# Kernel optimization log

Hardware: AMD Instinct MI355X
Metric: run time of the kernel (lower is better)

Reference implementation:

```python
import jax, jax.numpy as jnp
import numpy as np

N = 8192
C = 128
K = 20          # neighbors per dilation branch
DILS = (1, 2)   # dilations
K_FULL = K * max(DILS)  # neighbors in the base knn graph
R = 4           # upsampling ratio
N_IDGCN = 2     # inception blocks
NEG_SLOPE_CONV = 0.2
NEG_SLOPE_MLP = 0.01  # torch LeakyReLU default in reconstructor


def knn_idx(pos, k):
    # brute-force knn on [N,3]; exclude self by taking k+1 and dropping col 0
    sq = jnp.sum(pos * pos, axis=-1)                       # [N]
    d = sq[:, None] + sq[None, :] - 2.0 * (pos @ pos.T)    # [N,N]
    _, idx = jax.lax.top_k(-d, k + 1)                      # nearest first
    return idx[:, 1:]                                      # [N,k]


def edge_conv(x, idx, W, b):
    # EdgeConv: max_j LeakyReLU(W @ [x_i, x_j - x_i] + b)
    xj = x[idx]                                            # [N,k,C] gather
    xi = jnp.broadcast_to(x[:, None, :], xj.shape)
    e = jnp.concatenate([xi, xj - xi], axis=-1)            # [N,k,2C]
    h = jax.nn.leaky_relu(e @ W + b, NEG_SLOPE_CONV)
    return jnp.max(h, axis=1)                              # [N,Cout]


def setup_inputs() -> dict:
    key = jax.random.key(0)
    ks = jax.random.split(key, 10)
    s_lift = 1.0 / np.sqrt(6.0)
    s_gcn = 1.0 / np.sqrt(2.0 * C)
    s_mlp = 1.0 / np.sqrt(C)
    n_gcn = N_IDGCN * len(DILS)
    return {
        "x": jax.random.normal(ks[0], (N, 3), dtype=jnp.float32),
        "W0": jax.random.normal(ks[1], (6, C), dtype=jnp.float32) * s_lift,
        "b0": jnp.zeros((C,), dtype=jnp.float32),
        "Wg": jax.random.normal(ks[2], (n_gcn, 2 * C, C), dtype=jnp.float32) * s_gcn,
        "bg": jnp.zeros((n_gcn, C), dtype=jnp.float32),
        "Wu": jax.random.normal(ks[3], (2 * C, R * C), dtype=jnp.float32) * s_gcn,
        "bu": jnp.zeros((R * C,), dtype=jnp.float32),
        "Wr1": jax.random.normal(ks[4], (C, C), dtype=jnp.float32) * s_mlp,
        "br1": jnp.zeros((C,), dtype=jnp.float32),
        "Wr2": jax.random.normal(ks[5], (C, 3), dtype=jnp.float32) * s_mlp,
        "br2": jnp.zeros((3,), dtype=jnp.float32),
    }


def reference(x, W0, b0, Wg, bg, Wu, bu, Wr1, br1, Wr2, br2):
    pos = x
    # knn graph on positions (k * max(dilations) neighbors)
    idx = knn_idx(pos, K_FULL)                             # [N, K_FULL]
    # lift 3 -> C with an EdgeConv on the first K neighbors
    h = edge_conv(pos, idx[:, :K], W0, b0)                 # [N, C]
    # Inception DenseGCN feature extractor: dilated EdgeConv branches + residual
    li = 0
    for _ in range(N_IDGCN):
        acc = jnp.zeros_like(h)
        for d in DILS:
            idx_d = idx[:, ::d][:, :K]                     # dilated neighbors
            acc = acc + edge_conv(h, idx_d, Wg[li], bg[li])
            li += 1
        h = h + acc / float(len(DILS))                     # residual
    # NodeShuffle upsampler: EdgeConv to r*C then shuffle nodes
    u = edge_conv(h, idx[:, :K], Wu, bu)                   # [N, r*C]
    u = u.reshape(N * R, C)                                # [N*r, C]
    # reconstructor MLP -> 3D coordinates
    q = jax.nn.leaky_relu(u @ Wr1 + br1, NEG_SLOPE_MLP)
    q = q @ Wr2 + br2                                      # [N*r, 3]
    return q
```

## Files before the change

### kernel.cpp

```cpp
#include <hip/hip_runtime.h>
#include <math.h>

#define N_PTS 8192
#define KFULL 40
#define KNB 20
#define QB 8
#define KBLK 512
#define NBUCK 1024
#define CAP 384

typedef unsigned short u16;
typedef unsigned int u32;
typedef unsigned long long u64;
typedef __attribute__((ext_vector_type(8))) short bf16x8;
typedef __attribute__((ext_vector_type(4))) float f32x4;

__device__ __forceinline__ u16 f2b(float v) {
  u32 u = __float_as_uint(v);
  return (u16)((u + 0x7FFFu + ((u >> 16) & 1u)) >> 16);
}
__device__ __forceinline__ u32 pk2(float a, float b) {
  return (u32)f2b(a) | ((u32)f2b(b) << 16);
}
__device__ __forceinline__ u32 dmap(float d) {
  u32 b = __float_as_uint(d);
  return b ^ ((u32)(((int)b) >> 31) | 0x80000000u);
}
__device__ __forceinline__ void maxu4(const uint4 v, float m[8]) {
  m[0] = fmaxf(m[0], __uint_as_float(v.x << 16));
  m[1] = fmaxf(m[1], __uint_as_float(v.x & 0xFFFF0000u));
  m[2] = fmaxf(m[2], __uint_as_float(v.y << 16));
  m[3] = fmaxf(m[3], __uint_as_float(v.y & 0xFFFF0000u));
  m[4] = fmaxf(m[4], __uint_as_float(v.z << 16));
  m[5] = fmaxf(m[5], __uint_as_float(v.z & 0xFFFF0000u));
  m[6] = fmaxf(m[6], __uint_as_float(v.w << 16));
  m[7] = fmaxf(m[7], __uint_as_float(v.w & 0xFFFF0000u));
}
__device__ __forceinline__ void unp4(const uint4 v, float p[8]) {
  p[0] = __uint_as_float(v.x << 16);
  p[1] = __uint_as_float(v.x & 0xFFFF0000u);
  p[2] = __uint_as_float(v.y << 16);
  p[3] = __uint_as_float(v.y & 0xFFFF0000u);
  p[4] = __uint_as_float(v.z << 16);
  p[5] = __uint_as_float(v.z & 0xFFFF0000u);
  p[6] = __uint_as_float(v.w << 16);
  p[7] = __uint_as_float(v.w & 0xFFFF0000u);
}

typedef const __attribute__((address_space(1))) unsigned int* gas_p;
typedef __attribute__((address_space(3))) unsigned int* las_p;
__device__ __forceinline__ void gll16(const void* g, void* l) {
  __builtin_amdgcn_global_load_lds((gas_p)g, (las_p)l, 16, 0, 0);
}

__device__ __forceinline__ void scan_cut(const u32 (*hist)[NBUCK], int* s_cut,
                                         int t) {
  const int w = t >> 6, lane = t & 63;
  if (w < QB / 2) {
    const u32* H = hist[w];
    const int base = lane * (NBUCK / 64);
    u32 lsum = 0;
#pragma unroll
    for (int k = 0; k < NBUCK / 64; ++k) lsum += H[base + k];
    u32 inc = lsum;
#pragma unroll
    for (int off = 1; off < 64; off <<= 1) {
      const u32 u = __shfl_up(inc, off);
      if (lane >= off) inc += u;
    }
    const u32 excl = inc - lsum;
    const u32 TGT = KFULL + 1;
    const u32 exlo = excl & 0xFFFFu, inlo = inc & 0xFFFFu;
    if (exlo < TGT && inlo >= TGT) {
      u32 cum = exlo;
      for (int k = 0; k < NBUCK / 64; ++k) {
        cum += H[base + k] & 0xFFFFu;
        if (cum >= TGT) { s_cut[2 * w] = base + k; break; }
      }
    }
    const u32 exhi = excl >> 16, inhi = inc >> 16;
    if (exhi < TGT && inhi >= TGT) {
      u32 cum = exhi;
      for (int k = 0; k < NBUCK / 64; ++k) {
        cum += H[base + k] >> 16;
        if (cum >= TGT) { s_cut[2 * w + 1] = base + k; break; }
      }
    }
  }
}

__global__ __launch_bounds__(KBLK) void knn_kernel(const float4* __restrict__ pos4,
                                                   int* __restrict__ idx_out) {
  __shared__ __align__(16) u32 hmem[CAP * QB * 2];
  u32 (*hist)[NBUCK] = (u32(*)[NBUCK])hmem;
  u64 (*cand)[CAP] = (u64(*)[CAP])hmem;
  __shared__ float4 s_q[QB];
  __shared__ int s_cut[QB];
  __shared__ int s_cnt[QB];

  const int qb = blockIdx.x * QB, t = threadIdx.x;
  if (t < QB) {
    s_q[t] = pos4[qb + t];
    s_cnt[t] = 0;
  }
  for (int b = t; b < 4 * NBUCK; b += KBLK) hmem[b] = 0;
  __syncthreads();

  float qx[QB], qy[QB], qz[QB], qs[QB];
#pragma unroll
  for (int q = 0; q < QB; ++q) {
    const float4 v = s_q[q];
    qx[q] = -2.0f * v.x; qy[q] = -2.0f * v.y; qz[q] = -2.0f * v.z; qs[q] = v.w;
  }

  {
    const int j = t << 4;
    const float4 p = pos4[j];
#pragma unroll
    for (int q = 0; q < QB; ++q) {
      const float d = fmaf(qx[q], p.x, fmaf(qy[q], p.y, fmaf(qz[q], p.z, qs[q] + p.w)));
      const u32 bk = dmap(d) >> 22;
      atomicAdd(&hist[q >> 1][bk], 1u << ((q & 1) * 16));
    }
  }
  __syncthreads();
  scan_cut(hist, s_cut, t);
  __syncthreads();
  int bcut[QB];
#pragma unroll
  for (int q = 0; q < QB; ++q) bcut[q] = s_cut[q];
  for (int b = t; b < 4 * NBUCK; b += KBLK) hmem[b] = 0;
  __syncthreads();

#pragma unroll 2
  for (int s = 0; s < 16; ++s) {
    const int j = t + (s << 9);
    const float4 p = pos4[j];
#pragma unroll
    for (int q = 0; q < QB; ++q) {
      const float d = fmaf(qx[q], p.x, fmaf(qy[q], p.y, fmaf(qz[q], p.z, qs[q] + p.w)));
      const u32 bk = dmap(d) >> 22;
      if ((int)bk <= bcut[q]) atomicAdd(&hist[q >> 1][bk], 1u << ((q & 1) * 16));
    }
  }
  __syncthreads();
  scan_cut(hist, s_cut, t);
  __syncthreads();
#pragma unroll
  for (int q = 0; q < QB; ++q) bcut[q] = s_cut[q];
  __syncthreads();

#pragma unroll 2
  for (int s = 0; s < 16; ++s) {
    const int j = t + (s << 9);
    const float4 p = pos4[j];
#pragma unroll
    for (int q = 0; q < QB; ++q) {
      const float d = fmaf(qx[q], p.x, fmaf(qy[q], p.y, fmaf(qz[q], p.z, qs[q] + p.w)));
      const u32 mp = dmap(d);
      if ((int)(mp >> 22) <= bcut[q]) {
        const int slot = atomicAdd(&s_cnt[q], 1);
        if (slot < CAP) cand[q][slot] = ((u64)mp << 13) | (u64)j;
      }
    }
  }
  __syncthreads();

  {
    const int w = t >> 6, lane = t & 63;
    const int cnt = s_cnt[w] < CAP ? s_cnt[w] : CAP;
    for (int c0 = lane; c0 < cnt; c0 += 64) {
      const u64 my = cand[w][c0];
      int rank = 0;
      for (int c = 0; c < cnt; ++c) rank += (cand[w][c] < my) ? 1 : 0;
      if (rank >= 1 && rank <= KFULL)
        idx_out[(qb + w) * KFULL + (rank - 1)] = (int)(my & 0x1FFFull);
    }
  }
}

__device__ __forceinline__ void wcvt_body(const float* __restrict__ src,
                                          u16* __restrict__ dst, int ncols,
                                          int rows_per_tensor, int elems_per_tensor,
                                          int rg, int k) {
  const int li = rg / rows_per_tensor;
  const int r = rg % rows_per_tensor;
  const float* s = src + (size_t)li * elems_per_tensor;
  u16* d = dst + (size_t)li * elems_per_tensor;
  const int part = r / ncols, col = r % ncols;
  d[(size_t)r * 128 + k] = f2b(s[(size_t)(part * 128 + k) * ncols + col]);
}

__global__ __launch_bounds__(128) void prep_kernel(
    const float* __restrict__ x, const float* __restrict__ W0,
    const float* __restrict__ b0, const float* __restrict__ Wg,
    const float* __restrict__ Wu, const float* __restrict__ Wr1,
    float* __restrict__ Aout, u16* __restrict__ Pout, u16* __restrict__ Wgb,
    u16* __restrict__ Wub, u16* __restrict__ Wr1b, float4* __restrict__ pos4) {
  const int b = blockIdx.x, t = threadIdx.x;
  if (b < 8192) {
    const float px = x[b * 3 + 0], py = x[b * 3 + 1], pz = x[b * 3 + 2];
    const float a = b0[t] + px * W0[t] + py * W0[128 + t] + pz * W0[256 + t];
    const float p = px * W0[384 + t] + py * W0[512 + t] + pz * W0[640 + t];
    Aout[(size_t)b * 128 + t] = a;
    Pout[(size_t)b * 128 + t] = f2b(p);
  } else if (b < 9216) {
    wcvt_body(Wg, Wgb, 128, 256, 256 * 128, b - 8192, t);
  } else if (b < 10240) {
    wcvt_body(Wu, Wub, 512, 1024, 1024 * 128, b - 9216, t);
  } else if (b < 10368) {
    wcvt_body(Wr1, Wr1b, 128, 128, 128 * 128, b - 10240, t);
  } else {
    const int j = (b - 10368) * 128 + t;
    const float px = x[j * 3 + 0], py = x[j * 3 + 1], pz = x[j * 3 + 2];
    pos4[j] = make_float4(px, py, pz, px * px + py * py + pz * pz);
  }
}

__global__ __launch_bounds__(256) void gemm_mfma_kernel(
    const u16* __restrict__ Ain, const u16* __restrict__ Wt,
    const float* __restrict__ bias, int GA, int span_shift, int nAtot, int nPtot,
    float slope, int use_act, float* __restrict__ Aout, u16* __restrict__ Pout) {
  __shared__ __align__(16) u16 Al[128 * 128];
  __shared__ __align__(16) u16 Bl[64 * 128];
  const int bm = blockIdx.x * 128;
  const int bn = blockIdx.y * 64;
  const int tid = threadIdx.x;

#pragma unroll
  for (int it = 0; it < 8; ++it) {
    const int g = it * 256 + tid;
    const int row = g >> 4, cc = g & 15;
    const int sc = cc ^ (row & 7);
    gll16(Ain + (size_t)(bm + row) * 128 + sc * 8, &Al[g * 8]);
  }
#pragma unroll
  for (int it = 0; it < 4; ++it) {
    const int g = it * 256 + tid;
    const int row = g >> 4, cc = g & 15;
    const int sc = cc ^ (row & 7);
    gll16(Wt + (size_t)(bn + row) * 128 + sc * 8, &Bl[g * 8]);
  }
  __syncthreads();

  const int wv = tid >> 6, lane = tid & 63;
  const int wm = wv & 1, wn = wv >> 1;
  const int lr = lane & 15, lk = lane >> 4;

  bf16x8 a[4][4], b[2][4];
  f32x4 acc[4][2];
#pragma unroll
  for (int m = 0; m < 4; ++m)
#pragma unroll
    for (int n = 0; n < 2; ++n) acc[m][n] = (f32x4){0.f, 0.f, 0.f, 0.f};

#pragma unroll
  for (int m = 0; m < 4; ++m) {
    const int row = wm * 64 + m * 16 + lr;
#pragma unroll
    for (int ks = 0; ks < 4; ++ks) {
      const int c = ks * 4 + lk;
      a[m][ks] = *(const bf16x8*)&Al[row * 128 + (c ^ (row & 7)) * 8];
    }
  }
#pragma unroll
  for (int n = 0; n < 2; ++n) {
    const int col = wn * 32 + n * 16 + lr;
#pragma unroll
    for (int ks = 0; ks < 4; ++ks) {
      const int c = ks * 4 + lk;
      b[n][ks] = *(const bf16x8*)&Bl[col * 128 + (c ^ (col & 7)) * 8];
    }
  }

#pragma unroll
  for (int ks = 0; ks < 4; ++ks)
#pragma unroll
    for (int m = 0; m < 4; ++m)
#pragma unroll
      for (int n = 0; n < 2; ++n)
        acc[m][n] = __builtin_amdgcn_mfma_f32_16x16x32_bf16(a[m][ks], b[n][ks],
                                                            acc[m][n], 0, 0, 0);

  const int span = 1 << span_shift;
  const int GP = span - GA;
#pragma unroll
  for (int n = 0; n < 2; ++n) {
    const int col = bn + wn * 32 + n * 16 + lr;
    const int g = col >> span_shift;
    const int wi = col & (span - 1);
    const bool isA = wi < GA;
    const float bv = isA ? bias[g * GA + wi] : 0.f;
#pragma unroll
    for (int m = 0; m < 4; ++m) {
      const int row0 = bm + wm * 64 + m * 16 + lk * 4;
#pragma unroll
      for (int r = 0; r < 4; ++r) {
        float v = acc[m][n][r] + bv;
        if (isA) {
          if (use_act) v = v > 0.f ? v : v * slope;
          Aout[(size_t)(row0 + r) * nAtot + g * GA + wi] = v;
        } else {
          Pout[(size_t)(row0 + r) * nPtot + g * GP + (wi - GA)] = f2b(v);
        }
      }
    }
  }
}

__global__ __launch_bounds__(256) void gather_one_kernel(
    const float* __restrict__ A, const u16* __restrict__ P,
    const int* __restrict__ idx, int C, int dil, float* __restrict__ outf,
    u16* __restrict__ outb) {
  const int t = threadIdx.x;
  const int i = blockIdx.x * 16 + (t >> 4);
  const int c = blockIdx.y * 128 + (t & 15) * 8;
  float m[8];
#pragma unroll
  for (int k = 0; k < 8; ++k) m[k] = -INFINITY;
  const int ib = i * KFULL;
#pragma unroll
  for (int j = 0; j < KNB; ++j) {
    const int n = idx[ib + j * dil] & (N_PTS - 1);
    maxu4(*(const uint4*)&P[(size_t)n * C + c], m);
  }
  float pv[8];
  unp4(*(const uint4*)&P[(size_t)i * C + c], pv);
  const float4 a0 = *(const float4*)&A[(size_t)i * C + c];
  const float4 a1 = *(const float4*)&A[(size_t)i * C + c + 4];
  const float av[8] = {a0.x, a0.y, a0.z, a0.w, a1.x, a1.y, a1.z, a1.w};
  float v[8];
#pragma unroll
  for (int k = 0; k < 8; ++k) {
    const float x = av[k] - pv[k] + m[k];
    v[k] = x > 0.f ? x : 0.2f * x;
  }
  if (outf) {
    *(float4*)&outf[(size_t)i * C + c] = make_float4(v[0], v[1], v[2], v[3]);
    *(float4*)&outf[(size_t)i * C + c + 4] = make_float4(v[4], v[5], v[6], v[7]);
  }
  if (outb) {
    uint4 pb = {pk2(v[0], v[1]), pk2(v[2], v[3]), pk2(v[4], v[5]), pk2(v[6], v[7])};
    *(uint4*)&outb[(size_t)i * C + c] = pb;
  }
}

__global__ __launch_bounds__(256) void gather_pair_kernel(
    const float* __restrict__ Ap, const u16* __restrict__ Pp,
    const int* __restrict__ idx, float* __restrict__ h, u16* __restrict__ hb) {
  const int t = threadIdx.x;
  const int i = blockIdx.x * 16 + (t >> 4);
  const int c = (t & 15) * 8;
  float m1[8], m2[8];
#pragma unroll
  for (int k = 0; k < 8; ++k) { m1[k] = -INFINITY; m2[k] = -INFINITY; }
  const int ib = i * KFULL;
#pragma unroll
  for (int j = 0; j < KNB; ++j) {
    const int n1 = idx[ib + j] & (N_PTS - 1);
    maxu4(*(const uint4*)&Pp[(size_t)n1 * 256 + c], m1);
    const int n2 = idx[ib + 2 * j] & (N_PTS - 1);
    maxu4(*(const uint4*)&Pp[(size_t)n2 * 256 + 128 + c], m2);
  }
  float p0[8], p1[8];
  unp4(*(const uint4*)&Pp[(size_t)i * 256 + c], p0);
  unp4(*(const uint4*)&Pp[(size_t)i * 256 + 128 + c], p1);
  const float4 a00 = *(const float4*)&Ap[(size_t)i * 256 + c];
  const float4 a01 = *(const float4*)&Ap[(size_t)i * 256 + c + 4];
  const float4 a10 = *(const float4*)&Ap[(size_t)i * 256 + 128 + c];
  const float4 a11 = *(const float4*)&Ap[(size_t)i * 256 + 128 + c + 4];
  const float av0[8] = {a00.x, a00.y, a00.z, a00.w, a01.x, a01.y, a01.z, a01.w};
  const float av1[8] = {a10.x, a10.y, a10.z, a10.w, a11.x, a11.y, a11.z, a11.w};
  const float4 h0 = *(const float4*)&h[(size_t)i * 128 + c];
  const float4 h1 = *(const float4*)&h[(size_t)i * 128 + c + 4];
  const float hv[8] = {h0.x, h0.y, h0.z, h0.w, h1.x, h1.y, h1.z, h1.w};
  float v[8];
#pragma unroll
  for (int k = 0; k < 8; ++k) {
    float x1 = av0[k] - p0[k] + m1[k];
    x1 = x1 > 0.f ? x1 : 0.2f * x1;
    float x2 = av1[k] - p1[k] + m2[k];
    x2 = x2 > 0.f ? x2 : 0.2f * x2;
    v[k] = hv[k] + 0.5f * (x1 + x2);
  }
  *(float4*)&h[(size_t)i * 128 + c] = make_float4(v[0], v[1], v[2], v[3]);
  *(float4*)&h[(size_t)i * 128 + c + 4] = make_float4(v[4], v[5], v[6], v[7]);
  uint4 pb = {pk2(v[0], v[1]), pk2(v[2], v[3]), pk2(v[4], v[5]), pk2(v[6], v[7])};
  *(uint4*)&hb[(size_t)i * 128 + c] = pb;
}

__global__ __launch_bounds__(128) void recon2_kernel(const float* __restrict__ T,
                                                     const float* __restrict__ Wr2,
                                                     const float* __restrict__ br2,
                                                     float* __restrict__ out) {
  __shared__ float tile[32][129];
  __shared__ float w2[384];
  const int tid = threadIdx.x;
  const int r0 = blockIdx.x * 32;
  w2[tid] = Wr2[tid];
  w2[tid + 128] = Wr2[tid + 128];
  w2[tid + 256] = Wr2[tid + 256];
  for (int s = 0; s < 32; ++s) tile[s][tid] = T[(size_t)(r0 + s) * 128 + tid];
  __syncthreads();
  if (tid < 96) {
    const int r = tid / 3, n = tid % 3;
    float acc = br2[n];
#pragma unroll
    for (int k = 0; k < 128; ++k) acc = fmaf(tile[r][k], w2[k * 3 + n], acc);
    out[(size_t)(r0 + r) * 3 + n] = acc;
  }
}

extern "C" void kernel_launch(void* const* d_in, const int* in_sizes, int n_in,
                              void* d_out, int out_size, void* d_ws, size_t ws_size,
                              hipStream_t stream) {
  const float* x = (const float*)d_in[0];
  const float* W0 = (const float*)d_in[1];
  const float* b0 = (const float*)d_in[2];
  const float* Wg = (const float*)d_in[3];
  const float* bg = (const float*)d_in[4];
  const float* Wu = (const float*)d_in[5];
  const float* bu = (const float*)d_in[6];
  const float* Wr1 = (const float*)d_in[7];
  const float* br1 = (const float*)d_in[8];
  const float* Wr2 = (const float*)d_in[9];
  const float* br2 = (const float*)d_in[10];
  float* out = (float*)d_out;

  char* w = (char*)d_ws;
  int* idx = (int*)(w + 0);
  float4* pos4 = (float4*)(w + 1310720);
  float* h = (float*)(w + 1441792);
  u16* hb = (u16*)(w + 5636096);
  float* Apair = (float*)(w + 7733248);
  u16* Ppair = (u16*)(w + 16121856);
  u16* Wgb = (u16*)(w + 20316160);
  u16* Wub = (u16*)(w + 20578304);
  u16* Wr1b = (u16*)(w + 20840448);
  float* Abig = (float*)(w + 20873216);
  u16* Pbig = (u16*)(w + 37650432);
  u16* Ub = (u16*)Apair;
  float* T = Abig;

  prep_kernel<<<10432, 128, 0, stream>>>(x, W0, b0, Wg, Wu, Wr1, Abig, Pbig, Wgb,
                                         Wub, Wr1b, pos4);

  knn_kernel<<<N_PTS / QB, KBLK, 0, stream>>>(pos4, idx);

  gather_one_kernel<<<dim3(512, 1), 256, 0, stream>>>(Abig, Pbig, idx, 128, 1, h, hb);

  for (int blk = 0; blk < 2; ++blk) {
    const int li = blk * 2;
    gemm_mfma_kernel<<<dim3(64, 8), 256, 0, stream>>>(
        hb, Wgb + (size_t)li * 256 * 128, bg + li * 128, 128, 8, 256, 256, 0.f, 0,
        Apair, Ppair);
    gather_pair_kernel<<<512, 256, 0, stream>>>(Apair, Ppair, idx, h, hb);
  }

  gemm_mfma_kernel<<<dim3(64, 16), 256, 0, stream>>>(hb, Wub, bu, 512, 10, 512, 512,
                                                     0.f, 0, Abig, Pbig);
  gather_one_kernel<<<dim3(512, 4), 256, 0, stream>>>(Abig, Pbig, idx, 512, 1,
                                                      (float*)nullptr, Ub);

  gemm_mfma_kernel<<<dim3(256, 2), 256, 0, stream>>>(Ub, Wr1b, br1, 128, 7, 128, 128,
                                                     0.01f, 1, T, (u16*)nullptr);
  recon2_kernel<<<1024, 128, 0, stream>>>(T, Wr2, br2, out);
}
```

Before: 166.3 us.

## Replace brute-force kNN scan with uniform-grid spatial binning

Points are binned into a 16x16x16 uniform grid with count, scan and scatter kernels that build sorted positions and a permutation. Each wave then handles one query. It first estimates a radius from a 1/8 subsample histogram, then scans only grid cells within that radius to refine the histogram cut and collect candidates. This replaces the full N×N distance passes, at the cost of three extra small launches, one-query-per-wave imbalance, and radius-dependent cell loops.

```diff
diff --git a/kernel.cpp b/kernel.cpp
--- a/kernel.cpp
+++ b/kernel.cpp
@@ -4,10 +4,9 @@
 #define N_PTS 8192
 #define KFULL 40
 #define KNB 20
-#define QB 8
-#define KBLK 512
-#define NBUCK 1024
+#define NBK 1024
 #define CAP 384
+#define GR 16
 
 typedef unsigned short u16;
 typedef unsigned int u32;
@@ -25,6 +24,16 @@
 __device__ __forceinline__ u32 dmap(float d) {
   u32 b = __float_as_uint(d);
   return b ^ ((u32)(((int)b) >> 31) | 0x80000000u);
+}
+__device__ __forceinline__ float inv_edge(int b) {
+  if (b >= 1022) return 3.4e38f;
+  const u32 m = (((u32)(b + 1)) << 22) - 1u;
+  if (m < 0x80000000u) return 0.f;
+  return __uint_as_float(m - 0x80000000u);
+}
+__device__ __forceinline__ int cellc(float x) {
+  int c = (int)floorf((x + 5.0f) * 1.6f);
+  return c < 0 ? 0 : (c > 15 ? 15 : c);
 }
 __device__ __forceinline__ void maxu4(const uint4 v, float m[8]) {
   m[0] = fmaxf(m[0], __uint_as_float(v.x << 16));
@@ -53,129 +62,158 @@
   __builtin_amdgcn_global_load_lds((gas_p)g, (las_p)l, 16, 0, 0);
 }
 
-__device__ __forceinline__ void scan_cut(const u32 (*hist)[NBUCK], int* s_cut,
-                                         int t) {
-  const int w = t >> 6, lane = t & 63;
-  if (w < QB / 2) {
-    const u32* H = hist[w];
-    const int base = lane * (NBUCK / 64);
-    u32 lsum = 0;
-#pragma unroll
-    for (int k = 0; k < NBUCK / 64; ++k) lsum += H[base + k];
-    u32 inc = lsum;
-#pragma unroll
-    for (int off = 1; off < 64; off <<= 1) {
-      const u32 u = __shfl_up(inc, off);
-      if (lane >= off) inc += u;
+__global__ __launch_bounds__(512) void cell_count_kernel(const float4* __restrict__ pos4,
+                                                         int* __restrict__ cellcnt) {
+  const int j = blockIdx.x * 512 + threadIdx.x;
+  const float4 p = pos4[j];
+  const int cid = (cellc(p.x) << 8) | (cellc(p.y) << 4) | cellc(p.z);
+  atomicAdd(&cellcnt[cid], 1);
+}
+
+__global__ __launch_bounds__(1024) void cell_scan_kernel(const int* __restrict__ cnt,
+                                                         int* __restrict__ start) {
+  __shared__ int wsum[16];
+  const int t = threadIdx.x, lane = t & 63, w = t >> 6;
+  const int c0 = cnt[t * 4], c1 = cnt[t * 4 + 1], c2 = cnt[t * 4 + 2], c3 = cnt[t * 4 + 3];
+  const int s = c0 + c1 + c2 + c3;
+  int inc = s;
+#pragma unroll
+  for (int off = 1; off < 64; off <<= 1) {
+    const int u = __shfl_up(inc, off);
+    if (lane >= off) inc += u;
+  }
+  if (lane == 63) wsum[w] = inc;
+  __syncthreads();
+  int wpre = 0;
+  for (int k = 0; k < w; ++k) wpre += wsum[k];
+  const int excl = wpre + inc - s;
+  start[t * 4] = excl;
+  start[t * 4 + 1] = excl + c0;
+  start[t * 4 + 2] = excl + c0 + c1;
+  start[t * 4 + 3] = excl + c0 + c1 + c2;
+  if (t == 1023) start[4096] = excl + s;
+}
+
+__global__ __launch_bounds__(512) void cell_scatter_kernel(
+    const float4* __restrict__ pos4, const int* __restrict__ cellstart,
+    int* __restrict__ fill, float4* __restrict__ pos4s, int* __restrict__ perm) {
+  const int j = blockIdx.x * 512 + threadIdx.x;
+  const float4 p = pos4[j];
+  const int cid = (cellc(p.x) << 8) | (cellc(p.y) << 4) | cellc(p.z);
+  const int slot = cellstart[cid] + atomicAdd(&fill[cid], 1);
+  pos4s[slot] = p;
+  perm[slot] = j;
+}
+
+__device__ __forceinline__ int scan_cut_wave(const u32* H, int lane) {
+  const int base = lane * 16;
+  u32 lsum = 0;
+#pragma unroll
+  for (int k = 0; k < 16; ++k) lsum += H[base + k];
+  u32 inc = lsum;
+#pragma unroll
+  for (int off = 1; off < 64; off <<= 1) {
+    const u32 u = __shfl_up(inc, off);
+    if (lane >= off) inc += u;
+  }
+  const u32 excl = inc - lsum;
+  int cut = -1;
+  if (excl < 41u && inc >= 41u) {
+    u32 cum = excl;
+    for (int k = 0; k < 16; ++k) {
+      cum += H[base + k];
+      if (cum >= 41u) { cut = base + k; break; }
     }
-    const u32 excl = inc - lsum;
-    const u32 TGT = KFULL + 1;
-    const u32 exlo = excl & 0xFFFFu, inlo = inc & 0xFFFFu;
-    if (exlo < TGT && inlo >= TGT) {
-      u32 cum = exlo;
-      for (int k = 0; k < NBUCK / 64; ++k) {
-        cum += H[base + k] & 0xFFFFu;
-        if (cum >= TGT) { s_cut[2 * w] = base + k; break; }
+  }
+  const u64 mask = __ballot(cut >= 0);
+  if (mask == 0ull) return NBK - 1;
+  const int src = __ffsll((long long)mask) - 1;
+  return __shfl(cut, src);
+}
+
+__global__ __launch_bounds__(512) void knn_kernel(const float4* __restrict__ pos4s,
+                                                  const int* __restrict__ perm,
+                                                  const int* __restrict__ cellstart,
+                                                  int* __restrict__ idx_out) {
+  __shared__ __align__(16) u32 hist[8][NBK];
+  u64 (*cand)[CAP] = (u64(*)[CAP])hist;
+  __shared__ int s_cnt[8];
+
+  const int t = threadIdx.x, w = t >> 6, lane = t & 63;
+  const int qslot = blockIdx.x * 8 + w;
+  const float4 q = pos4s[qslot];
+  const float ax = -2.0f * q.x, ay = -2.0f * q.y, az = -2.0f * q.z, aw = q.w;
+
+  for (int b = lane; b < NBK; b += 64) hist[w][b] = 0;
+  if (lane == 0) s_cnt[w] = 0;
+  __syncthreads();
+
+#pragma unroll 4
+  for (int j = lane; j < 1024; j += 64) {
+    const float4 p = pos4s[j * 8];
+    const float d = fmaf(ax, p.x, fmaf(ay, p.y, fmaf(az, p.z, aw + p.w)));
+    atomicAdd(&hist[w][dmap(d) >> 22], 1u);
+  }
+  __syncthreads();
+  const int bc0 = scan_cut_wave(hist[w], lane);
+  const float R2a = fmaxf(inv_edge(bc0), 0.f);
+  __syncthreads();
+  for (int b = lane; b < NBK; b += 64) hist[w][b] = 0;
+  __syncthreads();
+
+  {
+    const float R = sqrtf(R2a) * 1.0001f + 1e-6f;
+    const int cxlo = cellc(q.x - R), cxhi = cellc(q.x + R);
+    const int cylo = cellc(q.y - R), cyhi = cellc(q.y + R);
+    const int czlo = cellc(q.z - R), czhi = cellc(q.z + R);
+    for (int cx = cxlo; cx <= cxhi; ++cx)
+      for (int cy = cylo; cy <= cyhi; ++cy) {
+        const int base = (cx << 8) | (cy << 4);
+        const int js = cellstart[base | czlo];
+        const int je = cellstart[(base | czhi) + 1];
+        for (int j = js + lane; j < je; j += 64) {
+          const float4 p = pos4s[j];
+          const float d = fmaf(ax, p.x, fmaf(ay, p.y, fmaf(az, p.z, aw + p.w)));
+          if (d <= R2a) atomicAdd(&hist[w][dmap(d) >> 22], 1u);
+        }
       }
-    }
-    const u32 exhi = excl >> 16, inhi = inc >> 16;
-    if (exhi < TGT && inhi >= TGT) {
-      u32 cum = exhi;
-      for (int k = 0; k < NBUCK / 64; ++k) {
-        cum += H[base + k] >> 16;
-        if (cum >= TGT) { s_cut[2 * w + 1] = base + k; break; }
+  }
+  __syncthreads();
+  const int bc1 = scan_cut_wave(hist[w], lane);
+  const float R2b = fmaxf(inv_edge(bc1), 0.f);
+  __syncthreads();
+
+  {
+    const float R = sqrtf(R2b) * 1.0001f + 1e-6f;
+    const int cxlo = cellc(q.x - R), cxhi = cellc(q.x + R);
+    const int cylo = cellc(q.y - R), cyhi = cellc(q.y + R);
+    const int czlo = cellc(q.z - R), czhi = cellc(q.z + R);
+    for (int cx = cxlo; cx <= cxhi; ++cx)
+      for (int cy = cylo; cy <= cyhi; ++cy) {
+        const int base = (cx << 8) | (cy << 4);
+        const int js = cellstart[base | czlo];
+        const int je = cellstart[(base | czhi) + 1];
+        for (int j = js + lane; j < je; j += 64) {
+          const float4 p = pos4s[j];
+          const float d = fmaf(ax, p.x, fmaf(ay, p.y, fmaf(az, p.z, aw + p.w)));
+          if (d <= R2b) {
+            const int slot = atomicAdd(&s_cnt[w], 1);
+            if (slot < CAP)
+              cand[w][slot] = ((u64)dmap(d) << 13) | (u64)perm[j];
+          }
+        }
       }
-    }
-  }
-}
-
-__global__ __launch_bounds__(KBLK) void knn_kernel(const float4* __restrict__ pos4,
-                                                   int* __restrict__ idx_out) {
-  __shared__ __align__(16) u32 hmem[CAP * QB * 2];
-  u32 (*hist)[NBUCK] = (u32(*)[NBUCK])hmem;
-  u64 (*cand)[CAP] = (u64(*)[CAP])hmem;
-  __shared__ float4 s_q[QB];
-  __shared__ int s_cut[QB];
-  __shared__ int s_cnt[QB];
-
-  const int qb = blockIdx.x * QB, t = threadIdx.x;
-  if (t < QB) {
-    s_q[t] = pos4[qb + t];
-    s_cnt[t] = 0;
-  }
-  for (int b = t; b < 4 * NBUCK; b += KBLK) hmem[b] = 0;
-  __syncthreads();
-
-  float qx[QB], qy[QB], qz[QB], qs[QB];
-#pragma unroll
-  for (int q = 0; q < QB; ++q) {
-    const float4 v = s_q[q];
-    qx[q] = -2.0f * v.x; qy[q] = -2.0f * v.y; qz[q] = -2.0f * v.z; qs[q] = v.w;
-  }
-
-  {
-    const int j = t << 4;
-    const float4 p = pos4[j];
-#pragma unroll
-    for (int q = 0; q < QB; ++q) {
-      const float d = fmaf(qx[q], p.x, fmaf(qy[q], p.y, fmaf(qz[q], p.z, qs[q] + p.w)));
-      const u32 bk = dmap(d) >> 22;
-      atomicAdd(&hist[q >> 1][bk], 1u << ((q & 1) * 16));
-    }
-  }
-  __syncthreads();
-  scan_cut(hist, s_cut, t);
-  __syncthreads();
-  int bcut[QB];
-#pragma unroll
-  for (int q = 0; q < QB; ++q) bcut[q] = s_cut[q];
-  for (int b = t; b < 4 * NBUCK; b += KBLK) hmem[b] = 0;
-  __syncthreads();
-
-#pragma unroll 2
-  for (int s = 0; s < 16; ++s) {
-    const int j = t + (s << 9);
-    const float4 p = pos4[j];
-#pragma unroll
-    for (int q = 0; q < QB; ++q) {
-      const float d = fmaf(qx[q], p.x, fmaf(qy[q], p.y, fmaf(qz[q], p.z, qs[q] + p.w)));
-      const u32 bk = dmap(d) >> 22;
-      if ((int)bk <= bcut[q]) atomicAdd(&hist[q >> 1][bk], 1u << ((q & 1) * 16));
-    }
-  }
-  __syncthreads();
-  scan_cut(hist, s_cut, t);
-  __syncthreads();
-#pragma unroll
-  for (int q = 0; q < QB; ++q) bcut[q] = s_cut[q];
-  __syncthreads();
-
-#pragma unroll 2
-  for (int s = 0; s < 16; ++s) {
-    const int j = t + (s << 9);
-    const float4 p = pos4[j];
-#pragma unroll
-    for (int q = 0; q < QB; ++q) {
-      const float d = fmaf(qx[q], p.x, fmaf(qy[q], p.y, fmaf(qz[q], p.z, qs[q] + p.w)));
-      const u32 mp = dmap(d);
-      if ((int)(mp >> 22) <= bcut[q]) {
-        const int slot = atomicAdd(&s_cnt[q], 1);
-        if (slot < CAP) cand[q][slot] = ((u64)mp << 13) | (u64)j;
-      }
-    }
-  }
-  __syncthreads();
-
-  {
-    const int w = t >> 6, lane = t & 63;
-    const int cnt = s_cnt[w] < CAP ? s_cnt[w] : CAP;
-    for (int c0 = lane; c0 < cnt; c0 += 64) {
-      const u64 my = cand[w][c0];
-      int rank = 0;
-      for (int c = 0; c < cnt; ++c) rank += (cand[w][c] < my) ? 1 : 0;
-      if (rank >= 1 && rank <= KFULL)
-        idx_out[(qb + w) * KFULL + (rank - 1)] = (int)(my & 0x1FFFull);
-    }
+  }
+  __syncthreads();
+
+  const int cnt = s_cnt[w] < CAP ? s_cnt[w] : CAP;
+  const int orig_q = perm[qslot];
+  for (int c0 = lane; c0 < cnt; c0 += 64) {
+    const u64 my = cand[w][c0];
+    int rank = 0;
+    for (int c = 0; c < cnt; ++c) rank += (cand[w][c] < my) ? 1 : 0;
+    if (rank >= 1 && rank <= KFULL)
+      idx_out[orig_q * KFULL + (rank - 1)] = (int)(my & 0x1FFFull);
   }
 }
 
@@ -196,7 +234,8 @@
     const float* __restrict__ b0, const float* __restrict__ Wg,
     const float* __restrict__ Wu, const float* __restrict__ Wr1,
     float* __restrict__ Aout, u16* __restrict__ Pout, u16* __restrict__ Wgb,
-    u16* __restrict__ Wub, u16* __restrict__ Wr1b, float4* __restrict__ pos4) {
+    u16* __restrict__ Wub, u16* __restrict__ Wr1b, float4* __restrict__ pos4,
+    int* __restrict__ cellcnt) {
   const int b = blockIdx.x, t = threadIdx.x;
   if (b < 8192) {
     const float px = x[b * 3 + 0], py = x[b * 3 + 1], pz = x[b * 3 + 2];
@@ -210,10 +249,12 @@
     wcvt_body(Wu, Wub, 512, 1024, 1024 * 128, b - 9216, t);
   } else if (b < 10368) {
     wcvt_body(Wr1, Wr1b, 128, 128, 128 * 128, b - 10240, t);
-  } else {
+  } else if (b < 10432) {
     const int j = (b - 10368) * 128 + t;
     const float px = x[j * 3 + 0], py = x[j * 3 + 1], pz = x[j * 3 + 2];
     pos4[j] = make_float4(px, py, pz, px * px + py * py + pz * pz);
+  } else {
+    cellcnt[(b - 10432) * 128 + t] = 0;
   }
 }
 
@@ -439,13 +480,21 @@
   u16* Wr1b = (u16*)(w + 20840448);
   float* Abig = (float*)(w + 20873216);
   u16* Pbig = (u16*)(w + 37650432);
+  float4* pos4s = (float4*)(w + 46039040);
+  int* perm = (int*)(w + 46170112);
+  int* cellstart = (int*)(w + 46202880);
+  int* cellcnt = (int*)(w + 46219520);
+  int* fill = (int*)(w + 46235904);
   u16* Ub = (u16*)Apair;
   float* T = Abig;
 
-  prep_kernel<<<10432, 128, 0, stream>>>(x, W0, b0, Wg, Wu, Wr1, Abig, Pbig, Wgb,
-                                         Wub, Wr1b, pos4);
-
-  knn_kernel<<<N_PTS / QB, KBLK, 0, stream>>>(pos4, idx);
+  prep_kernel<<<10496, 128, 0, stream>>>(x, W0, b0, Wg, Wu, Wr1, Abig, Pbig, Wgb,
+                                         Wub, Wr1b, pos4, cellcnt);
+
+  cell_count_kernel<<<16, 512, 0, stream>>>(pos4, cellcnt);
+  cell_scan_kernel<<<1, 1024, 0, stream>>>(cellcnt, cellstart);
+  cell_scatter_kernel<<<16, 512, 0, stream>>>(pos4, cellstart, fill, pos4s, perm);
+  knn_kernel<<<1024, 512, 0, stream>>>(pos4s, perm, cellstart, idx);
 
   gather_one_kernel<<<dim3(512, 1), 256, 0, stream>>>(Abig, Pbig, idx, 128, 1, h, hb);
 
```

Result: slower. 197.7 us (+18.9%).

## Replace two-pass histogram kNN selection with sampled radius bound plus fallback

Applied to the files above, without the earlier changes.

The kNN kernel builds its first histogram from a larger strided sample (2048 points instead of 512), turns the resulting bucket cut into a float distance threshold, and collects candidates directly in one full pass. This removes the second full-histogram pass and its scan and syncs. Candidate capacity rises to 512. A per-wave fallback rebuilds an exact histogram and recompacts candidates with ballot when the sampled bound lets too many through. The fallback is serial per query and slow if triggered, and sample-based cuts may leave fewer than K+1 candidates for some queries.

```diff
diff --git a/kernel.cpp b/kernel.cpp
--- a/kernel.cpp
+++ b/kernel.cpp
@@ -6,8 +6,8 @@
 #define KNB 20
 #define QB 8
 #define KBLK 512
-#define NBUCK 1024
-#define CAP 384
+#define NBK 1024
+#define CAP 512
 
 typedef unsigned short u16;
 typedef unsigned int u32;
@@ -25,6 +25,12 @@
 __device__ __forceinline__ u32 dmap(float d) {
   u32 b = __float_as_uint(d);
   return b ^ ((u32)(((int)b) >> 31) | 0x80000000u);
+}
+__device__ __forceinline__ float inv_edge(int b) {
+  if (b >= 1022) return 3.4e38f;
+  const u32 m = (((u32)(b + 1)) << 22) - 1u;
+  if (m < 0x80000000u) return 0.f;
+  return __uint_as_float(m - 0x80000000u);
 }
 __device__ __forceinline__ void maxu4(const uint4 v, float m[8]) {
   m[0] = fmaxf(m[0], __uint_as_float(v.x << 16));
@@ -53,15 +59,15 @@
   __builtin_amdgcn_global_load_lds((gas_p)g, (las_p)l, 16, 0, 0);
 }
 
-__device__ __forceinline__ void scan_cut(const u32 (*hist)[NBUCK], int* s_cut,
+__device__ __forceinline__ void scan_cut(const u32 (*hist)[NBK], int* s_cut,
                                          int t) {
   const int w = t >> 6, lane = t & 63;
   if (w < QB / 2) {
     const u32* H = hist[w];
-    const int base = lane * (NBUCK / 64);
+    const int base = lane * (NBK / 64);
     u32 lsum = 0;
 #pragma unroll
-    for (int k = 0; k < NBUCK / 64; ++k) lsum += H[base + k];
+    for (int k = 0; k < NBK / 64; ++k) lsum += H[base + k];
     u32 inc = lsum;
 #pragma unroll
     for (int off = 1; off < 64; off <<= 1) {
@@ -73,7 +79,7 @@
     const u32 exlo = excl & 0xFFFFu, inlo = inc & 0xFFFFu;
     if (exlo < TGT && inlo >= TGT) {
       u32 cum = exlo;
-      for (int k = 0; k < NBUCK / 64; ++k) {
+      for (int k = 0; k < NBK / 64; ++k) {
         cum += H[base + k] & 0xFFFFu;
         if (cum >= TGT) { s_cut[2 * w] = base + k; break; }
       }
@@ -81,7 +87,7 @@
     const u32 exhi = excl >> 16, inhi = inc >> 16;
     if (exhi < TGT && inhi >= TGT) {
       u32 cum = exhi;
-      for (int k = 0; k < NBUCK / 64; ++k) {
+      for (int k = 0; k < NBK / 64; ++k) {
         cum += H[base + k] >> 16;
         if (cum >= TGT) { s_cut[2 * w + 1] = base + k; break; }
       }
@@ -89,10 +95,36 @@
   }
 }
 
+__device__ __forceinline__ int scan_cut_wave(const u32* H, int lane) {
+  const int base = lane * (NBK / 64);
+  u32 lsum = 0;
+#pragma unroll
+  for (int k = 0; k < NBK / 64; ++k) lsum += H[base + k];
+  u32 inc = lsum;
+#pragma unroll
+  for (int off = 1; off < 64; off <<= 1) {
+    const u32 u = __shfl_up(inc, off);
+    if (lane >= off) inc += u;
+  }
+  const u32 excl = inc - lsum;
+  int cut = -1;
+  if (excl < 41u && inc >= 41u) {
+    u32 cum = excl;
+    for (int k = 0; k < NBK / 64; ++k) {
+      cum += H[base + k];
+      if (cum >= 41u) { cut = base + k; break; }
+    }
+  }
+  const u64 mask = __ballot(cut >= 0);
+  if (mask == 0ull) return NBK - 1;
+  const int src = __ffsll((long long)mask) - 1;
+  return __shfl(cut, src);
+}
+
 __global__ __launch_bounds__(KBLK) void knn_kernel(const float4* __restrict__ pos4,
                                                    int* __restrict__ idx_out) {
-  __shared__ __align__(16) u32 hmem[CAP * QB * 2];
-  u32 (*hist)[NBUCK] = (u32(*)[NBUCK])hmem;
+  __shared__ __align__(16) u32 hmem[2 * QB * CAP];
+  u32 (*hist)[NBK] = (u32(*)[NBK])hmem;
   u64 (*cand)[CAP] = (u64(*)[CAP])hmem;
   __shared__ float4 s_q[QB];
   __shared__ int s_cut[QB];
@@ -103,7 +135,7 @@
     s_q[t] = pos4[qb + t];
     s_cnt[t] = 0;
   }
-  for (int b = t; b < 4 * NBUCK; b += KBLK) hmem[b] = 0;
+  for (int b = t; b < 4 * NBK; b += KBLK) hmem[b] = 0;
   __syncthreads();
 
   float qx[QB], qy[QB], qz[QB], qs[QB];
@@ -113,24 +145,22 @@
     qx[q] = -2.0f * v.x; qy[q] = -2.0f * v.y; qz[q] = -2.0f * v.z; qs[q] = v.w;
   }
 
-  {
-    const int j = t << 4;
+#pragma unroll
+  for (int s = 0; s < 4; ++s) {
+    const int j = (t + (s << 9)) << 2;
     const float4 p = pos4[j];
 #pragma unroll
     for (int q = 0; q < QB; ++q) {
       const float d = fmaf(qx[q], p.x, fmaf(qy[q], p.y, fmaf(qz[q], p.z, qs[q] + p.w)));
-      const u32 bk = dmap(d) >> 22;
-      atomicAdd(&hist[q >> 1][bk], 1u << ((q & 1) * 16));
+      atomicAdd(&hist[q >> 1][dmap(d) >> 22], 1u << ((q & 1) * 16));
     }
   }
   __syncthreads();
   scan_cut(hist, s_cut, t);
   __syncthreads();
-  int bcut[QB];
-#pragma unroll
-  for (int q = 0; q < QB; ++q) bcut[q] = s_cut[q];
-  for (int b = t; b < 4 * NBUCK; b += KBLK) hmem[b] = 0;
-  __syncthreads();
+  float r2[QB];
+#pragma unroll
+  for (int q = 0; q < QB; ++q) r2[q] = inv_edge(s_cut[q]);
 
 #pragma unroll 2
   for (int s = 0; s < 16; ++s) {
@@ -139,28 +169,9 @@
 #pragma unroll
     for (int q = 0; q < QB; ++q) {
       const float d = fmaf(qx[q], p.x, fmaf(qy[q], p.y, fmaf(qz[q], p.z, qs[q] + p.w)));
-      const u32 bk = dmap(d) >> 22;
-      if ((int)bk <= bcut[q]) atomicAdd(&hist[q >> 1][bk], 1u << ((q & 1) * 16));
-    }
-  }
-  __syncthreads();
-  scan_cut(hist, s_cut, t);
-  __syncthreads();
-#pragma unroll
-  for (int q = 0; q < QB; ++q) bcut[q] = s_cut[q];
-  __syncthreads();
-
-#pragma unroll 2
-  for (int s = 0; s < 16; ++s) {
-    const int j = t + (s << 9);
-    const float4 p = pos4[j];
-#pragma unroll
-    for (int q = 0; q < QB; ++q) {
-      const float d = fmaf(qx[q], p.x, fmaf(qy[q], p.y, fmaf(qz[q], p.z, qs[q] + p.w)));
-      const u32 mp = dmap(d);
-      if ((int)(mp >> 22) <= bcut[q]) {
+      if (d <= r2[q]) {
         const int slot = atomicAdd(&s_cnt[q], 1);
-        if (slot < CAP) cand[q][slot] = ((u64)mp << 13) | (u64)j;
+        if (slot < CAP) cand[q][slot] = ((u64)dmap(d) << 13) | (u64)j;
       }
     }
   }
@@ -168,11 +179,42 @@
 
   {
     const int w = t >> 6, lane = t & 63;
-    const int cnt = s_cnt[w] < CAP ? s_cnt[w] : CAP;
-    for (int c0 = lane; c0 < cnt; c0 += 64) {
+    int cnt = s_cnt[w];
+    if (cnt > CAP) {
+      const float4 qv = s_q[w];
+      const float ax = -2.0f * qv.x, ay = -2.0f * qv.y, az = -2.0f * qv.z;
+      const float aw = qv.w;
+      const float R2w = inv_edge(s_cut[w]);
+      u32* fbh = (u32*)cand[w];
+      for (int b = lane; b < NBK; b += 64) fbh[b] = 0;
+      for (int j = lane; j < N_PTS; j += 64) {
+        const float4 p = pos4[j];
+        const float d = fmaf(ax, p.x, fmaf(ay, p.y, fmaf(az, p.z, aw + p.w)));
+        if (d <= R2w) atomicAdd(&fbh[dmap(d) >> 22], 1u);
+      }
+      const int cut2 = scan_cut_wave(fbh, lane);
+      const float R2r = inv_edge(cut2);
+      int base = 0;
+      for (int j0 = 0; j0 < N_PTS; j0 += 64) {
+        const int j = j0 + lane;
+        const float4 p = pos4[j];
+        const float d = fmaf(ax, p.x, fmaf(ay, p.y, fmaf(az, p.z, aw + p.w)));
+        const bool pred = (d <= R2r);
+        const u64 mask = __ballot(pred);
+        if (pred) {
+          const int off = __popcll(mask & ((1ull << lane) - 1ull));
+          if (base + off < CAP)
+            cand[w][base + off] = ((u64)dmap(d) << 13) | (u64)j;
+        }
+        base += (int)__popcll(mask);
+      }
+      cnt = base;
+    }
+    const int cmax = cnt < CAP ? cnt : CAP;
+    for (int c0 = lane; c0 < cmax; c0 += 64) {
       const u64 my = cand[w][c0];
       int rank = 0;
-      for (int c = 0; c < cnt; ++c) rank += (cand[w][c] < my) ? 1 : 0;
+      for (int c = 0; c < cmax; ++c) rank += (cand[w][c] < my) ? 1 : 0;
       if (rank >= 1 && rank <= KFULL)
         idx_out[(qb + w) * KFULL + (rank - 1)] = (int)(my & 0x1FFFull);
     }
```

New measurement: 221.1 us. 1.33x slower.
